# Kernel tuning notes

Measured on AMD Instinct MI355X. Metric: run time of the kernel, lower is better.

The kernel has to match this reference:

```python
import jax, jax.numpy as jnp
import numpy as np

D = 1024
H = 16
HD = D // H
B = 4
L = 2048
FFN = 4 * D
EPS = 1e-5


def _layer_norm(x, g, b):
    mu = jnp.mean(x, axis=-1, keepdims=True)
    var = jnp.mean(jnp.square(x - mu), axis=-1, keepdims=True)
    return (x - mu) * jax.lax.rsqrt(var + EPS) * g + b


def setup_inputs() -> dict:
    key = jax.random.key(0)
    ks = jax.random.split(key, 16)
    s = 1.0 / np.sqrt(D)
    inp = {
        "x": jax.random.normal(ks[0], (B, L, D), dtype=jnp.float32),
        "rel_pos_bias": jax.random.normal(ks[1], (1, H, L, L), dtype=jnp.float32) * 0.02,
        "wq": jax.random.normal(ks[2], (D, D), dtype=jnp.float32) * s,
        "bq": jnp.zeros((D,), jnp.float32),
        "wk": jax.random.normal(ks[3], (D, D), dtype=jnp.float32) * s,
        "bk": jnp.zeros((D,), jnp.float32),
        "wv": jax.random.normal(ks[4], (D, D), dtype=jnp.float32) * s,
        "bv": jnp.zeros((D,), jnp.float32),
        "wo": jax.random.normal(ks[5], (D, D), dtype=jnp.float32) * s,
        "bo": jnp.zeros((D,), jnp.float32),
        "g1": jnp.ones((D,), jnp.float32),
        "be1": jnp.zeros((D,), jnp.float32),
        "g2": jnp.ones((D,), jnp.float32),
        "be2": jnp.zeros((D,), jnp.float32),
        "w1": jax.random.normal(ks[6], (D, FFN), dtype=jnp.float32) * s,
        "bf1": jnp.zeros((FFN,), jnp.float32),
        "w2": jax.random.normal(ks[7], (FFN, D), dtype=jnp.float32) * (1.0 / np.sqrt(FFN)),
        "bf2": jnp.zeros((D,), jnp.float32),
    }
    return inp


def reference(x, rel_pos_bias, wq, bq, wk, bk, wv, bv, wo, bo,
              g1, be1, g2, be2, w1, bf1, w2, bf2):
    scale = HD ** -0.5
    residual = x
    xn = _layer_norm(x, g1, be1)
    # projections -> (B, H, L, HD)
    q = (xn @ wq + bq).reshape(B, L, H, HD).transpose(0, 2, 1, 3)
    k = (xn @ wk + bk).reshape(B, L, H, HD).transpose(0, 2, 1, 3)
    v = (xn @ wv + bv).reshape(B, L, H, HD).transpose(0, 2, 1, 3)
    scores = jnp.einsum('bhqd,bhkd->bhqk', q, k) * scale
    causal = jnp.tril(jnp.ones((L, L), dtype=bool))
    scores = jnp.where(causal[None, None], scores, -jnp.inf)
    scores = scores + rel_pos_bias
    attn = jax.nn.softmax(scores, axis=-1)
    out = jnp.einsum('bhqk,bhkd->bhqd', attn, v)
    out = out.transpose(0, 2, 1, 3).reshape(B, L, D)
    out = out @ wo + bo
    x = residual + out
    residual = x
    xn = _layer_norm(x, g2, be2)
    h = jax.nn.relu(xn @ w1 + bf1)
    x = residual + (h @ w2 + bf2)
    return x
```

## Files before the change

### kernel.cpp

```cpp
#include <hip/hip_runtime.h>
#include <hip/hip_bf16.h>

#define D_   1024
#define H_   16
#define HD_  64
#define B_   4
#define L_   2048
#define FFN_ 4096
#define M_   (B_ * L_)

typedef __bf16 bf16x8 __attribute__((ext_vector_type(8)));
typedef float f32x4 __attribute__((ext_vector_type(4)));
typedef unsigned short ushort8 __attribute__((ext_vector_type(8)));
typedef unsigned short ushort4v __attribute__((ext_vector_type(4)));

__device__ inline unsigned short f2bf(float f) {
    unsigned int u = __float_as_uint(f);
    u += 0x7fff + ((u >> 16) & 1);
    return (unsigned short)(u >> 16);
}
__device__ inline float bf2f(unsigned short u) {
    return __uint_as_float(((unsigned int)u) << 16);
}

__global__ __launch_bounds__(256) void k_transpose_bf16(
    const float* __restrict__ in, unsigned short* __restrict__ out, int K, int N)
{
    __shared__ float tile[64][65];
    int k0 = blockIdx.y * 64, n0 = blockIdx.x * 64;
    int t = threadIdx.x;
    int r = t >> 2, cs = (t & 3) * 16;
    const float* src = in + (size_t)(k0 + r) * N + n0 + cs;
#pragma unroll
    for (int i = 0; i < 16; i += 4) {
        float4 v = *(const float4*)(src + i);
        tile[r][cs + i + 0] = v.x;
        tile[r][cs + i + 1] = v.y;
        tile[r][cs + i + 2] = v.z;
        tile[r][cs + i + 3] = v.w;
    }
    __syncthreads();
    unsigned short* dst = out + (size_t)(n0 + r) * K + k0 + cs;
#pragma unroll
    for (int i = 0; i < 16; ++i) dst[i] = f2bf(tile[cs + i][r]);
}

__global__ void k_concat_bias(const float* __restrict__ bq, const float* __restrict__ bk,
                              const float* __restrict__ bv, float* __restrict__ out)
{
    int i = blockIdx.x * 256 + threadIdx.x;
    float v = (i < 1024) ? bq[i] : (i < 2048 ? bk[i - 1024] : bv[i - 2048]);
    out[i] = v;
}

__global__ __launch_bounds__(256) void k_layernorm(
    const float* __restrict__ x, const float* __restrict__ g, const float* __restrict__ be,
    unsigned short* __restrict__ out)
{
    int row = blockIdx.x;
    const float* xr = x + (size_t)row * D_;
    int t = threadIdx.x;
    float4 v = *(const float4*)(xr + t * 4);
    float s = v.x + v.y + v.z + v.w;
    float sq = v.x * v.x + v.y * v.y + v.z * v.z + v.w * v.w;
#pragma unroll
    for (int off = 32; off >= 1; off >>= 1) {
        s  += __shfl_down(s, off);
        sq += __shfl_down(sq, off);
    }
    __shared__ float ps[4], psq[4];
    int w = t >> 6;
    if ((t & 63) == 0) { ps[w] = s; psq[w] = sq; }
    __syncthreads();
    float tot  = ps[0] + ps[1] + ps[2] + ps[3];
    float totq = psq[0] + psq[1] + psq[2] + psq[3];
    float mu  = tot * (1.f / D_);
    float var = totq * (1.f / D_) - mu * mu;
    float inv = rsqrtf(var + 1e-5f);
    float4 gv = *(const float4*)(g + t * 4);
    float4 bv = *(const float4*)(be + t * 4);
    ushort4v o;
    o[0] = f2bf((v.x - mu) * inv * gv.x + bv.x);
    o[1] = f2bf((v.y - mu) * inv * gv.y + bv.y);
    o[2] = f2bf((v.z - mu) * inv * gv.z + bv.z);
    o[3] = f2bf((v.w - mu) * inv * gv.w + bv.w);
    *(ushort4v*)(out + (size_t)row * D_ + t * 4) = o;
}

template <bool OUT_BF16, bool RELU, bool RESID>
__global__ __launch_bounds__(256, 2) void k_gemm(
    const unsigned short* __restrict__ A, const unsigned short* __restrict__ Bt,
    const float* __restrict__ bias, const float* __restrict__ resid,
    void* __restrict__ Cout, int M, int N, int K)
{
    __shared__ unsigned short sA[128 * 40];
    __shared__ unsigned short sB[128 * 40];
    int m0 = blockIdx.y * 128, n0 = blockIdx.x * 128;
    int tid = threadIdx.x, lane = tid & 63, wvi = tid >> 6;
    int wm = (wvi & 1) * 64, wn = (wvi >> 1) * 64;
    int lr = lane & 15, qd = lane >> 4;

    f32x4 acc[4][4] = {};

    int sr = tid >> 2, ss = (tid & 3) * 8;
    const unsigned short* pA0 = A  + (size_t)(m0 + sr)      * K + ss;
    const unsigned short* pA1 = A  + (size_t)(m0 + 64 + sr) * K + ss;
    const unsigned short* pB0 = Bt + (size_t)(n0 + sr)      * K + ss;
    const unsigned short* pB1 = Bt + (size_t)(n0 + 64 + sr) * K + ss;

    for (int k0 = 0; k0 < K; k0 += 32) {
        ushort8 a0 = *(const ushort8*)(pA0 + k0);
        ushort8 a1 = *(const ushort8*)(pA1 + k0);
        ushort8 b0 = *(const ushort8*)(pB0 + k0);
        ushort8 b1 = *(const ushort8*)(pB1 + k0);
        if (k0) __syncthreads();
        *(ushort8*)(sA + sr * 40 + ss)        = a0;
        *(ushort8*)(sA + (64 + sr) * 40 + ss) = a1;
        *(ushort8*)(sB + sr * 40 + ss)        = b0;
        *(ushort8*)(sB + (64 + sr) * 40 + ss) = b1;
        __syncthreads();
        bf16x8 af[4], bfr[4];
#pragma unroll
        for (int i = 0; i < 4; ++i)
            af[i] = *(const bf16x8*)(sA + (wm + i * 16 + lr) * 40 + qd * 8);
#pragma unroll
        for (int i = 0; i < 4; ++i)
            bfr[i] = *(const bf16x8*)(sB + (wn + i * 16 + lr) * 40 + qd * 8);
#pragma unroll
        for (int mi = 0; mi < 4; ++mi)
#pragma unroll
            for (int ni = 0; ni < 4; ++ni)
                acc[mi][ni] = __builtin_amdgcn_mfma_f32_16x16x32_bf16(
                    af[mi], bfr[ni], acc[mi][ni], 0, 0, 0);
    }

#pragma unroll
    for (int ni = 0; ni < 4; ++ni) {
        int col = n0 + wn + ni * 16 + lr;
        float bvv = bias[col];
#pragma unroll
        for (int mi = 0; mi < 4; ++mi) {
#pragma unroll
            for (int r = 0; r < 4; ++r) {
                int row = m0 + wm + mi * 16 + qd * 4 + r;
                float v = acc[mi][ni][r] + bvv;
                if (RELU) v = fmaxf(v, 0.f);
                if (RESID) v += resid[(size_t)row * N + col];
                if (OUT_BF16)
                    ((unsigned short*)Cout)[(size_t)row * N + col] = f2bf(v);
                else
                    ((float*)Cout)[(size_t)row * N + col] = v;
            }
        }
    }
}

__global__ __launch_bounds__(256, 4) void k_attn(
    const unsigned short* __restrict__ qkv, const float* __restrict__ rpb,
    unsigned short* __restrict__ out)
{
    __shared__ unsigned short Ks[64 * 72];
    __shared__ unsigned short Vt[64 * 64];
    __shared__ unsigned short Sp[64 * 72];

    int flat = blockIdx.x;
    int xcd = flat & 7, b = (flat >> 3) & 3, hi = flat >> 5;
    int g = hi * 8 + xcd;
    int h = g & 15;
    int qt = 31 - (g >> 4);
    int q0 = qt * 64;

    int t = threadIdx.x, lane = t & 63, w = t >> 6;
    int lr = lane & 15, qd = lane >> 4;
    int sr = t >> 2, ss = (t & 3) * 16;
    int bL = b * L_;

    bf16x8 aq[2];
    {
        const unsigned short* qsrc =
            qkv + (size_t)(bL + q0 + w * 16 + lr) * 3072 + h * 64 + qd * 8;
        aq[0] = *(const bf16x8*)qsrc;
        aq[1] = *(const bf16x8*)(qsrc + 32);
    }

    f32x4 oacc[4] = {};
    float m_r[4], l_r[4];
#pragma unroll
    for (int r = 0; r < 4; ++r) { m_r[r] = -1e30f; l_r[r] = 0.f; }

    int qrow_base = q0 + w * 16 + qd * 4;
    int ntile = qt + 1;

    ushort8 krA, krB, vrA, vrB;
    {
        const unsigned short* kb_ = qkv + (size_t)(bL + sr) * 3072 + 1024 + h * 64 + ss;
        krA = *(const ushort8*)kb_;  krB = *(const ushort8*)(kb_ + 8);
        vrA = *(const ushort8*)(kb_ + 1024); vrB = *(const ushort8*)(kb_ + 1032);
    }

    for (int kt = 0; kt < ntile; ++kt) {
        int k0 = kt * 64;
        if (kt) __syncthreads();

        *(ushort8*)(Ks + sr * 72 + ss)     = krA;
        *(ushort8*)(Ks + sr * 72 + ss + 8) = krB;

        {
            int role = sr & 1;
            int srp  = sr & ~1;
#pragma unroll
            for (int i = 0; i < 8; ++i) {
                int sendv = role ? (int)(unsigned int)vrA[i] : (int)(unsigned int)vrB[i];
                int got = __shfl_xor(sendv, 4);
                int d = role ? (ss + 8 + i) : (ss + i);
                unsigned short lo = role ? (unsigned short)got : vrA[i];
                unsigned short hi = role ? vrB[i] : (unsigned short)got;
                int swz = (d ^ (d >> 3)) & 7;
                unsigned int u = (unsigned int)lo | ((unsigned int)hi << 16);
                *(unsigned int*)(Vt + d * 64 + (srp ^ (swz << 3))) = u;
            }
        }
        __syncthreads();

        float rv[4][4];
        {
            const float* rpb_base = rpb + ((size_t)h * L_ + qrow_base) * L_ + k0;
#pragma unroll
            for (int r = 0; r < 4; ++r)
#pragma unroll
                for (int nt = 0; nt < 4; ++nt)
                    rv[r][nt] = rpb_base[(size_t)r * L_ + nt * 16 + lr];
        }

        if (kt + 1 < ntile) {
            const unsigned short* kb_ =
                qkv + (size_t)(bL + k0 + 64 + sr) * 3072 + 1024 + h * 64 + ss;
            krA = *(const ushort8*)kb_;  krB = *(const ushort8*)(kb_ + 8);
            vrA = *(const ushort8*)(kb_ + 1024); vrB = *(const ushort8*)(kb_ + 1032);
        }

        f32x4 sc4[4] = {};
#pragma unroll
        for (int ks = 0; ks < 2; ++ks) {
#pragma unroll
            for (int nt = 0; nt < 4; ++nt) {
                bf16x8 bk8 = *(const bf16x8*)(Ks + (nt * 16 + lr) * 72 + ks * 32 + qd * 8);
                sc4[nt] = __builtin_amdgcn_mfma_f32_16x16x32_bf16(aq[ks], bk8, sc4[nt], 0, 0, 0);
            }
        }

        float pvv[4][4], mx[4];
#pragma unroll
        for (int r = 0; r < 4; ++r) {
            mx[r] = -1e30f;
#pragma unroll
            for (int nt = 0; nt < 4; ++nt) {
                int kcol = k0 + nt * 16 + lr;
                float sv = sc4[nt][r] * 0.125f + rv[r][nt];
                if (kcol > qrow_base + r) sv = -1e30f;
                pvv[r][nt] = sv;
                mx[r] = fmaxf(mx[r], sv);
            }
        }
#pragma unroll
        for (int r = 0; r < 4; ++r) {
            mx[r] = fmaxf(mx[r], __shfl_xor(mx[r], 1));
            mx[r] = fmaxf(mx[r], __shfl_xor(mx[r], 2));
            mx[r] = fmaxf(mx[r], __shfl_xor(mx[r], 4));
            mx[r] = fmaxf(mx[r], __shfl_xor(mx[r], 8));
        }
#pragma unroll
        for (int r = 0; r < 4; ++r) {
            float mnew  = fmaxf(m_r[r], mx[r]);
            float alpha = __expf(m_r[r] - mnew);
            float psum = 0.f;
#pragma unroll
            for (int nt = 0; nt < 4; ++nt) {
                float p = __expf(pvv[r][nt] - mnew);
                psum += p;
                Sp[(w * 16 + qd * 4 + r) * 72 + nt * 16 + lr] = f2bf(p);
            }
            psum += __shfl_xor(psum, 1);
            psum += __shfl_xor(psum, 2);
            psum += __shfl_xor(psum, 4);
            psum += __shfl_xor(psum, 8);
            l_r[r] = l_r[r] * alpha + psum;
            m_r[r] = mnew;
            oacc[0][r] *= alpha; oacc[1][r] *= alpha;
            oacc[2][r] *= alpha; oacc[3][r] *= alpha;
        }

#pragma unroll
        for (int ks = 0; ks < 2; ++ks) {
            bf16x8 ap = *(const bf16x8*)(Sp + (w * 16 + lr) * 72 + ks * 32 + qd * 8);
#pragma unroll
            for (int dt = 0; dt < 4; ++dt) {
                int d = dt * 16 + lr;
                int swz = (d ^ (d >> 3)) & 7;
                bf16x8 bv8 = *(const bf16x8*)(Vt + d * 64 + ((ks * 32 + qd * 8) ^ (swz << 3)));
                oacc[dt] = __builtin_amdgcn_mfma_f32_16x16x32_bf16(ap, bv8, oacc[dt], 0, 0, 0);
            }
        }
    }

#pragma unroll
    for (int r = 0; r < 4; ++r) {
        float linv = 1.f / l_r[r];
        int qrow = q0 + w * 16 + qd * 4 + r;
        unsigned short* dst = out + (size_t)(bL + qrow) * 1024 + h * 64;
#pragma unroll
        for (int dt = 0; dt < 4; ++dt)
            dst[dt * 16 + lr] = f2bf(oacc[dt][r] * linv);
    }
}

extern "C" void kernel_launch(void* const* d_in, const int* in_sizes, int n_in,
                              void* d_out, int out_size, void* d_ws, size_t ws_size,
                              hipStream_t stream)
{
    const float* x   = (const float*)d_in[0];
    const float* rpb = (const float*)d_in[1];
    const float* wq  = (const float*)d_in[2];
    const float* bq  = (const float*)d_in[3];
    const float* wk  = (const float*)d_in[4];
    const float* bk  = (const float*)d_in[5];
    const float* wv  = (const float*)d_in[6];
    const float* bv  = (const float*)d_in[7];
    const float* wo  = (const float*)d_in[8];
    const float* bo  = (const float*)d_in[9];
    const float* g1  = (const float*)d_in[10];
    const float* be1 = (const float*)d_in[11];
    const float* g2  = (const float*)d_in[12];
    const float* be2 = (const float*)d_in[13];
    const float* w1  = (const float*)d_in[14];
    const float* bf1 = (const float*)d_in[15];
    const float* w2  = (const float*)d_in[16];
    const float* bf2 = (const float*)d_in[17];
    float* out = (float*)d_out;
    char* ws = (char*)d_ws;

    unsigned short* xn1   = (unsigned short*)(ws + 0);
    unsigned short* qkv   = (unsigned short*)(ws + 16777216);
    unsigned short* attno = (unsigned short*)(ws + 0);
    unsigned short* hbuf  = (unsigned short*)(ws + 0);
    float*          xmid  = (float*)(ws + 67108864);
    unsigned short* xn2   = (unsigned short*)(ws + 100663296);
    unsigned short* wqkvT = (unsigned short*)(ws + 117440512);
    unsigned short* woT   = (unsigned short*)(ws + 123731968);
    unsigned short* w1T   = (unsigned short*)(ws + 125829120);
    unsigned short* w2T   = (unsigned short*)(ws + 134217728);
    float*          bqkv  = (float*)(ws + 142606336);

    k_transpose_bf16<<<dim3(16, 16), 256, 0, stream>>>(wq, wqkvT,                1024, 1024);
    k_transpose_bf16<<<dim3(16, 16), 256, 0, stream>>>(wk, wqkvT + 1024 * 1024,  1024, 1024);
    k_transpose_bf16<<<dim3(16, 16), 256, 0, stream>>>(wv, wqkvT + 2048 * 1024,  1024, 1024);
    k_transpose_bf16<<<dim3(16, 16), 256, 0, stream>>>(wo, woT,                  1024, 1024);
    k_transpose_bf16<<<dim3(64, 16), 256, 0, stream>>>(w1, w1T,                  1024, 4096);
    k_transpose_bf16<<<dim3(16, 64), 256, 0, stream>>>(w2, w2T,                  4096, 1024);
    k_concat_bias<<<12, 256, 0, stream>>>(bq, bk, bv, bqkv);

    k_layernorm<<<M_, 256, 0, stream>>>(x, g1, be1, xn1);
    k_gemm<true, false, false><<<dim3(24, 64), 256, 0, stream>>>(
        xn1, wqkvT, bqkv, nullptr, qkv, M_, 3072, 1024);
    k_attn<<<dim3(2048), 256, 0, stream>>>(qkv, rpb, attno);
    k_gemm<false, false, true><<<dim3(8, 64), 256, 0, stream>>>(
        attno, woT, bo, x, xmid, M_, 1024, 1024);
    k_layernorm<<<M_, 256, 0, stream>>>(xmid, g2, be2, xn2);
    k_gemm<true, true, false><<<dim3(32, 64), 256, 0, stream>>>(
        xn2, w1T, bf1, nullptr, hbuf, M_, 4096, 1024);
    k_gemm<false, false, true><<<dim3(8, 64), 256, 0, stream>>>(
        hbuf, w2T, bf2, xmid, out, M_, 1024, 4096);
}
```

Baseline: 864.5 us.

## Double-buffer GEMM tiles via direct global-to-LDS loads; tune attention priority and masking

The GEMM now uses global_load_lds to copy A/B tiles straight into double-buffered shared memory, prefetching the next K-slice while MFMAs consume the current one. This removes the register staging and one of the two barriers per iteration. The unpadded 32-wide LDS rows may cause bank conflicts on fragment reads. In attention, s_setprio is raised around the MFMA blocks, the causal mask is evaluated only on the diagonal tile, and the occupancy hint is raised from 4 to 6 blocks, which may add register pressure or spills.

```diff
diff --git a/kernel.cpp b/kernel.cpp
--- a/kernel.cpp
+++ b/kernel.cpp
@@ -21,6 +21,12 @@
 }
 __device__ inline float bf2f(unsigned short u) {
     return __uint_as_float(((unsigned int)u) << 16);
+}
+
+__device__ inline void gl_lds16(const unsigned short* g, unsigned short* l) {
+    __builtin_amdgcn_global_load_lds(
+        (const __attribute__((address_space(1))) unsigned int*)g,
+        (__attribute__((address_space(3))) unsigned int*)l, 16, 0, 0);
 }
 
 __global__ __launch_bounds__(256) void k_transpose_bf16(
@@ -93,39 +99,47 @@
     const float* __restrict__ bias, const float* __restrict__ resid,
     void* __restrict__ Cout, int M, int N, int K)
 {
-    __shared__ unsigned short sA[128 * 40];
-    __shared__ unsigned short sB[128 * 40];
+    __shared__ unsigned short sA[2][128 * 32];
+    __shared__ unsigned short sB[2][128 * 32];
     int m0 = blockIdx.y * 128, n0 = blockIdx.x * 128;
-    int tid = threadIdx.x, lane = tid & 63, wvi = tid >> 6;
-    int wm = (wvi & 1) * 64, wn = (wvi >> 1) * 64;
+    int tid = threadIdx.x, lane = tid & 63, wv = tid >> 6;
+    int wm = (wv & 1) * 64, wn = (wv >> 1) * 64;
     int lr = lane & 15, qd = lane >> 4;
 
     f32x4 acc[4][4] = {};
 
-    int sr = tid >> 2, ss = (tid & 3) * 8;
-    const unsigned short* pA0 = A  + (size_t)(m0 + sr)      * K + ss;
-    const unsigned short* pA1 = A  + (size_t)(m0 + 64 + sr) * K + ss;
-    const unsigned short* pB0 = Bt + (size_t)(n0 + sr)      * K + ss;
-    const unsigned short* pB1 = Bt + (size_t)(n0 + 64 + sr) * K + ss;
-
-    for (int k0 = 0; k0 < K; k0 += 32) {
-        ushort8 a0 = *(const ushort8*)(pA0 + k0);
-        ushort8 a1 = *(const ushort8*)(pA1 + k0);
-        ushort8 b0 = *(const ushort8*)(pB0 + k0);
-        ushort8 b1 = *(const ushort8*)(pB1 + k0);
-        if (k0) __syncthreads();
-        *(ushort8*)(sA + sr * 40 + ss)        = a0;
-        *(ushort8*)(sA + (64 + sr) * 40 + ss) = a1;
-        *(ushort8*)(sB + sr * 40 + ss)        = b0;
-        *(ushort8*)(sB + (64 + sr) * 40 + ss) = b1;
+    int srow = lane >> 2;
+    int scol = (lane & 3) * 8;
+    const unsigned short* gA0 = A  + (size_t)(m0 + wv * 32 + srow) * K + scol;
+    const unsigned short* gA1 = A  + (size_t)(m0 + wv * 32 + 16 + srow) * K + scol;
+    const unsigned short* gB0 = Bt + (size_t)(n0 + wv * 32 + srow) * K + scol;
+    const unsigned short* gB1 = Bt + (size_t)(n0 + wv * 32 + 16 + srow) * K + scol;
+    int lbase0 = (wv * 32) * 32;
+    int lbase1 = (wv * 32 + 16) * 32;
+
+    gl_lds16(gA0, &sA[0][lbase0]);
+    gl_lds16(gA1, &sA[0][lbase1]);
+    gl_lds16(gB0, &sB[0][lbase0]);
+    gl_lds16(gB1, &sB[0][lbase1]);
+
+    int nk = K >> 5;
+    for (int ki = 0; ki < nk; ++ki) {
+        int cur = ki & 1;
         __syncthreads();
+        if (ki + 1 < nk) {
+            int k1 = (ki + 1) << 5;
+            gl_lds16(gA0 + k1, &sA[cur ^ 1][lbase0]);
+            gl_lds16(gA1 + k1, &sA[cur ^ 1][lbase1]);
+            gl_lds16(gB0 + k1, &sB[cur ^ 1][lbase0]);
+            gl_lds16(gB1 + k1, &sB[cur ^ 1][lbase1]);
+        }
         bf16x8 af[4], bfr[4];
 #pragma unroll
         for (int i = 0; i < 4; ++i)
-            af[i] = *(const bf16x8*)(sA + (wm + i * 16 + lr) * 40 + qd * 8);
+            af[i] = *(const bf16x8*)(&sA[cur][(wm + i * 16 + lr) * 32 + qd * 8]);
 #pragma unroll
         for (int i = 0; i < 4; ++i)
-            bfr[i] = *(const bf16x8*)(sB + (wn + i * 16 + lr) * 40 + qd * 8);
+            bfr[i] = *(const bf16x8*)(&sB[cur][(wn + i * 16 + lr) * 32 + qd * 8]);
 #pragma unroll
         for (int mi = 0; mi < 4; ++mi)
 #pragma unroll
@@ -155,7 +169,7 @@
     }
 }
 
-__global__ __launch_bounds__(256, 4) void k_attn(
+__global__ __launch_bounds__(256, 6) void k_attn(
     const unsigned short* __restrict__ qkv, const float* __restrict__ rpb,
     unsigned short* __restrict__ out)
 {
@@ -240,6 +254,7 @@
         }
 
         f32x4 sc4[4] = {};
+        __builtin_amdgcn_s_setprio(1);
 #pragma unroll
         for (int ks = 0; ks < 2; ++ks) {
 #pragma unroll
@@ -248,16 +263,17 @@
                 sc4[nt] = __builtin_amdgcn_mfma_f32_16x16x32_bf16(aq[ks], bk8, sc4[nt], 0, 0, 0);
             }
         }
-
+        __builtin_amdgcn_s_setprio(0);
+
+        bool last = (kt == qt);
         float pvv[4][4], mx[4];
 #pragma unroll
         for (int r = 0; r < 4; ++r) {
             mx[r] = -1e30f;
 #pragma unroll
             for (int nt = 0; nt < 4; ++nt) {
-                int kcol = k0 + nt * 16 + lr;
                 float sv = sc4[nt][r] * 0.125f + rv[r][nt];
-                if (kcol > qrow_base + r) sv = -1e30f;
+                if (last && (k0 + nt * 16 + lr > qrow_base + r)) sv = -1e30f;
                 pvv[r][nt] = sv;
                 mx[r] = fmaxf(mx[r], sv);
             }
@@ -290,6 +306,7 @@
             oacc[2][r] *= alpha; oacc[3][r] *= alpha;
         }
 
+        __builtin_amdgcn_s_setprio(1);
 #pragma unroll
         for (int ks = 0; ks < 2; ++ks) {
             bf16x8 ap = *(const bf16x8*)(Sp + (w * 16 + lr) * 72 + ks * 32 + qd * 8);
@@ -301,6 +318,7 @@
                 oacc[dt] = __builtin_amdgcn_mfma_f32_16x16x32_bf16(ap, bv8, oacc[dt], 0, 0, 0);
             }
         }
+        __builtin_amdgcn_s_setprio(0);
     }
 
 #pragma unroll
```

After: 1.114 ms. +28.8%, slower.
